# Kernel tuning notes

Measured on AMD Instinct MI355X. Metric: run time of the kernel, lower is better.

The kernel has to match this reference:

```python
import jax, jax.numpy as jnp
import numpy as np

EPS = 1e-5
NUM_HEADS = 8

def _inorm(x):
    # InstanceNorm1d (affine=False): normalize over last (length) axis per (B, C)
    m = x.mean(axis=-1, keepdims=True)
    v = x.var(axis=-1, keepdims=True)  # biased variance, as torch instance norm
    return (x - m) * jax.lax.rsqrt(v + EPS)

def setup_inputs() -> dict:
    key = jax.random.key(0)
    ks = jax.random.split(key, 12)
    B, Nl, HW = 4, 1024, 4096
    Cl, Cv, Ck, Cval, Cout = 512, 512, 256, 256, 256
    w = lambda k, shape: (jax.random.normal(k, shape, jnp.float32) * 0.02)
    return {
        "l": jax.random.normal(ks[0], (B, Nl, Cl), jnp.float32),
        "x": jax.random.normal(ks[1], (B, HW, Cv), jnp.float32),
        "Wq": w(ks[2], (Ck, Cl)),   "bq": w(ks[3], (Ck,)),
        "Wk": w(ks[4], (Ck, Cv)),   "bk": w(ks[5], (Ck,)),
        "Wv": w(ks[6], (Cval, Cv)), "bv": w(ks[7], (Cval,)),
        "Ww": w(ks[8], (Cout, Cval)), "bw": w(ks[9], (Cout,)),
    }

def reference(l, x, Wq, bq, Wk, bk, Wv, bv, Ww, bw):
    H = NUM_HEADS
    Ck = Wq.shape[0]
    Cv = Wv.shape[0]
    dk, dv = Ck // H, Cv // H
    B, Nl, _ = l.shape
    HW = x.shape[1]

    # 1x1 Conv1d == per-position linear
    q = jnp.einsum('blc,kc->blk', l, Wq) + bq                     # [B, Nl, Ck]
    k = jnp.einsum('bnc,kc->bkn', x, Wk) + bk[None, :, None]      # [B, Ck, HW]
    k = _inorm(k)                                                  # InstanceNorm over HW
    v = jnp.einsum('bnc,kc->bkn', x, Wv) + bv[None, :, None]      # [B, Cv, HW]

    q = q.reshape(B, Nl, H, dk).transpose(0, 2, 1, 3)             # [B, H, Nl, dk]
    k = k.reshape(B, H, dk, HW)                                   # [B, H, dk, HW]
    v = v.reshape(B, H, dv, HW)                                   # [B, H, dv, HW]

    sim = jnp.einsum('bhld,bhdn->bhln', q, k) * (Ck ** -0.5)      # [B, H, Nl, HW]
    att = jax.nn.softmax(sim, axis=-1)
    out = jnp.einsum('bhln,bhdn->bhld', att, v)                   # [B, H, Nl, dv]

    out = out.transpose(0, 2, 1, 3).reshape(B, Nl, Cv)            # [B, Nl, Cv]
    out = jnp.einsum('blc,oc->bol', out, Ww) + bw[None, :, None]  # [B, Cout, Nl]
    out = _inorm(out)                                              # InstanceNorm over Nl
    return out.transpose(0, 2, 1)                                  # [B, Nl, Cout]
```

## Files before the change

kernel.cpp:

```cpp
#include <hip/hip_runtime.h>

constexpr int Bn = 4, NL = 1024, HWn = 4096, NH = 8;

typedef __attribute__((ext_vector_type(8))) short bf16x8;
typedef __attribute__((ext_vector_type(4))) float f32x4;
#define MFMA16 __builtin_amdgcn_mfma_f32_16x16x32_bf16

extern "C" __device__ float __ocml_native_exp2_f32(float);

__device__ __forceinline__ float b2f(unsigned short u) {
  union { unsigned int i; float f; } x; x.i = ((unsigned int)u) << 16; return x.f;
}
__device__ __forceinline__ unsigned short f2b(float f) {
  union { float f; unsigned int i; } x; x.f = f;
  unsigned int r = x.i + 0x7fffu + ((x.i >> 16) & 1u);
  return (unsigned short)(r >> 16);
}

__device__ __forceinline__ void async_load16(const unsigned short* g, unsigned short* l) {
  __builtin_amdgcn_global_load_lds(
      (const __attribute__((address_space(1))) unsigned int*)g,
      (__attribute__((address_space(3))) unsigned int*)l, 16, 0, 0);
}

__global__ __launch_bounds__(256) void conv_bf16(const float* __restrict__ src,
    unsigned short* __restrict__ dst, int n)
{
  int i = (blockIdx.x * 256 + threadIdx.x) * 4;
  if (i < n) {
    float4 v = *(const float4*)(src + i);
    ushort4 o; o.x = f2b(v.x); o.y = f2b(v.y); o.z = f2b(v.z); o.w = f2b(v.w);
    *(ushort4*)(dst + i) = o;
  }
}

__global__ __launch_bounds__(256) void conv_w4(const float* __restrict__ Wk,
    const float* __restrict__ Wv, const float* __restrict__ Wq,
    const float* __restrict__ Ww,
    unsigned short* __restrict__ wkb, unsigned short* __restrict__ wvb,
    unsigned short* __restrict__ wqb,
    unsigned short* __restrict__ wwh, unsigned short* __restrict__ wwl)
{
  int i = (blockIdx.x * 256 + threadIdx.x) * 4;
  if (blockIdx.y == 3) {
    if (i >= 65536) return;
    float4 v = *(const float4*)(Ww + i);
    ushort4 hi, lo;
    hi.x = f2b(v.x); lo.x = f2b(v.x - b2f(hi.x));
    hi.y = f2b(v.y); lo.y = f2b(v.y - b2f(hi.y));
    hi.z = f2b(v.z); lo.z = f2b(v.z - b2f(hi.z));
    hi.w = f2b(v.w); lo.w = f2b(v.w - b2f(hi.w));
    *(ushort4*)(wwh + i) = hi;
    *(ushort4*)(wwl + i) = lo;
    return;
  }
  const float* src = blockIdx.y == 0 ? Wk : (blockIdx.y == 1 ? Wv : Wq);
  unsigned short* dst = blockIdx.y == 0 ? wkb : (blockIdx.y == 1 ? wvb : wqb);
  float4 v = *(const float4*)(src + i);
  ushort4 o; o.x = f2b(v.x); o.y = f2b(v.y); o.z = f2b(v.z); o.w = f2b(v.w);
  *(ushort4*)(dst + i) = o;
}

__global__ __launch_bounds__(256, 3) void gemm128(
    const unsigned short* __restrict__ xbf, const unsigned short* __restrict__ lbf,
    const unsigned short* __restrict__ wkb, const unsigned short* __restrict__ wvb,
    const unsigned short* __restrict__ wqb,
    const float* __restrict__ bk, const float* __restrict__ bv, const float* __restrict__ bq,
    unsigned short* __restrict__ khb, unsigned short* __restrict__ vhb,
    unsigned short* __restrict__ qbuf)
{
  __shared__ unsigned short As[2][4096];
  __shared__ unsigned short Bs[2][4096];
  const int id = blockIdx.x;
  const int mode = id < 256 ? 0 : (id < 512 ? 1 : 2);
  const int local = id - (mode == 0 ? 0 : (mode == 1 ? 256 : 512));
  const int rb = local >> 1, cb = local & 1;
  const int m0 = rb * 128, n0 = cb * 128;
  const unsigned short* A = (mode == 2) ? lbf : xbf;
  const unsigned short* W = (mode == 0) ? wkb : (mode == 1 ? wvb : wqb);
  const float* bias = (mode == 0) ? bk : (mode == 1 ? bv : bq);

  const int tid = threadIdx.x, w = tid >> 6, lane = tid & 63;
  const int quad = lane >> 4, l15 = lane & 15;
  const int wr = w >> 1, wc = w & 1;

  const int p0 = tid, p1 = tid + 256;
  const int am0 = p0 >> 2, ak0 = (p0 & 3) * 8;
  const int am1 = p1 >> 2, ak1 = (p1 & 3) * 8;

  f32x4 acc[4][4];
#pragma unroll
  for (int i = 0; i < 4; ++i)
#pragma unroll
    for (int j = 0; j < 4; ++j) acc[i][j] = (f32x4){0.f, 0.f, 0.f, 0.f};

  async_load16(A + (size_t)(m0 + am0) * 512 + ak0, &As[0][p0 * 8]);
  async_load16(A + (size_t)(m0 + am1) * 512 + ak1, &As[0][p1 * 8]);
  async_load16(W + (size_t)(n0 + am0) * 512 + ak0, &Bs[0][p0 * 8]);
  async_load16(W + (size_t)(n0 + am1) * 512 + ak1, &Bs[0][p1 * 8]);

  for (int kt = 0; kt < 16; ++kt) {
    const int cur = kt & 1;
    __syncthreads();
    if (kt < 15) {
      int k0 = (kt + 1) * 32;
      async_load16(A + (size_t)(m0 + am0) * 512 + k0 + ak0, &As[cur ^ 1][p0 * 8]);
      async_load16(A + (size_t)(m0 + am1) * 512 + k0 + ak1, &As[cur ^ 1][p1 * 8]);
      async_load16(W + (size_t)(n0 + am0) * 512 + k0 + ak0, &Bs[cur ^ 1][p0 * 8]);
      async_load16(W + (size_t)(n0 + am1) * 512 + k0 + ak1, &Bs[cur ^ 1][p1 * 8]);
    }
    bf16x8 af[4], bf[4];
#pragma unroll
    for (int fr = 0; fr < 4; ++fr)
      af[fr] = *(const bf16x8*)&As[cur][(wr * 64 + fr * 16 + l15) * 32 + quad * 8];
#pragma unroll
    for (int fc = 0; fc < 4; ++fc)
      bf[fc] = *(const bf16x8*)&Bs[cur][(wc * 64 + fc * 16 + l15) * 32 + quad * 8];
#pragma unroll
    for (int fr = 0; fr < 4; ++fr)
#pragma unroll
      for (int fc = 0; fc < 4; ++fc)
        acc[fr][fc] = MFMA16(af[fr], bf[fc], acc[fr][fc], 0, 0, 0);
  }

  float bb[4];
#pragma unroll
  for (int fc = 0; fc < 4; ++fc) bb[fc] = bias[n0 + wc * 64 + fc * 16 + l15];
  unsigned short* dst = (mode == 0) ? khb : (mode == 1 ? vhb : qbuf);
#pragma unroll
  for (int fr = 0; fr < 4; ++fr) {
#pragma unroll
    for (int fc = 0; fc < 4; ++fc) {
      int col = n0 + wc * 64 + fc * 16 + l15;
#pragma unroll
      for (int r = 0; r < 4; ++r) {
        int row = m0 + wr * 64 + fr * 16 + quad * 4 + r;
        unsigned short val = f2b(acc[fr][fc][r] + bb[fc]);
        if (mode == 2) {
          dst[(size_t)row * 256 + col] = val;
        } else {
          int b = row >> 12, n = row & 4095, h = col >> 5, d = col & 31;
          dst[((size_t)(b * 8 + h) * 4096 + n) * 32 + d] = val;
        }
      }
    }
  }
}

__global__ __launch_bounds__(256) void kvstats(const unsigned short* __restrict__ khb,
    const unsigned short* __restrict__ vhb,
    float* __restrict__ ksum, float* __restrict__ kss, float* __restrict__ vcs)
{
  const int which = blockIdx.x >> 5, bh = blockIdx.x & 31, seg = blockIdx.y;
  const int t = threadIdx.x, d = t & 31, g = t >> 5;
  __shared__ float rs[256], rss[256];
  if (which == 0) {
    const unsigned short* base = khb + (size_t)bh * 131072 + (size_t)seg * 512 * 32;
    float s = 0.f, ss = 0.f;
    for (int i = 0; i < 64; ++i) {
      float v = b2f(base[(size_t)(g + i * 8) * 32 + d]);
      s += v; ss += v * v;
    }
    rs[t] = s; rss[t] = ss;
    __syncthreads();
    if (t < 32) {
      float a = 0.f, b = 0.f;
      for (int g2 = 0; g2 < 8; ++g2) { a += rs[t + g2 * 32]; b += rss[t + g2 * 32]; }
      atomicAdd(&ksum[bh * 32 + t], a);
      atomicAdd(&kss[bh * 32 + t], b);
    }
  } else {
    const unsigned short* base = vhb + (size_t)bh * 131072 + (size_t)seg * 512 * 32;
    float s = 0.f;
    for (int i = 0; i < 64; ++i) s += b2f(base[(size_t)(g + i * 8) * 32 + d]);
    rs[t] = s;
    __syncthreads();
    if (t < 32) {
      float a = 0.f;
      for (int g2 = 0; g2 < 8; ++g2) a += rs[t + g2 * 32];
      vcs[seg * 1024 + bh * 32 + t] = a;
    }
  }
}

__global__ __launch_bounds__(256) void kfinal(const float* __restrict__ ksum,
    const float* __restrict__ kss, float* __restrict__ krstd)
{
  int i = blockIdx.x * 256 + threadIdx.x;
  float m = ksum[i] * (1.f / 4096.f);
  float var = kss[i] * (1.f / 4096.f) - m * m;
  krstd[i] = rsqrtf(var + 1e-5f);
}

__global__ __launch_bounds__(256) void vpack(const unsigned short* __restrict__ vh,
    unsigned short* __restrict__ vfrag)
{
  __shared__ unsigned short vt[256][42];
  const int bh = blockIdx.x >> 4, slab = blockIdx.x & 15;
  const unsigned short* src = vh + ((size_t)bh * 4096 + slab * 256) * 32;
  const int t = threadIdx.x;
#pragma unroll
  for (int i = 0; i < 4; ++i) {
    int p = i * 256 + t;
    int n = p >> 2, piece = p & 3;
    uint4 v = *(const uint4*)(src + (size_t)n * 32 + piece * 8);
    unsigned int* lrow = (unsigned int*)&vt[n][piece * 8];
    lrow[0] = v.x; lrow[1] = v.y; lrow[2] = v.z; lrow[3] = v.w;
  }
  __syncthreads();
#pragma unroll
  for (int i = 0; i < 4; ++i) {
    int op = i * 256 + t;
    int lanep = op & 63, rest = op >> 6;
    int dvt = rest & 1, kh2 = (rest >> 1) & 1, chunkl = rest >> 2;
    int lq = lanep >> 4, ll = lanep & 15;
    unsigned short o[8];
#pragma unroll
    for (int j = 0; j < 8; ++j) {
      int kappa = kh2 * 32 + lq * 8 + j;
      int nloc = (kappa >> 2) + 16 * (kappa & 3);
      o[j] = vt[chunkl * 64 + nloc][dvt * 16 + ll];
    }
    size_t dst = ((((size_t)bh * 64 + slab * 4 + chunkl) * 2 + kh2) * 2 + dvt) * 512 + lanep * 8;
    *(bf16x8*)(vfrag + dst) = *(const bf16x8*)o;
  }
}

__global__ __launch_bounds__(256, 4) void attn6(const unsigned short* __restrict__ qbuf,
    const unsigned short* __restrict__ khb, const unsigned short* __restrict__ vfrag,
    const float* __restrict__ krstd, const float* __restrict__ vcs,
    float* __restrict__ po, float* __restrict__ pd)
{
  const int bh = blockIdx.x, b = bh >> 3, h = bh & 7;
  const int lsuper = blockIdx.y, quarter = blockIdx.z;
  const int tid = threadIdx.x, w = tid >> 6, lane = tid & 63;
  const int quad = lane >> 4, l15 = lane & 15;

  __shared__ unsigned short kb_s[2][2048];
  __shared__ unsigned short vb_s[2][2048];
  __shared__ unsigned short ps[4][2][16][72];

  bf16x8 qa[2];
  {
    float fold[8];
    const float* rp = krstd + bh * 32 + quad * 8;
#pragma unroll
    for (int j = 0; j < 8; ++j) fold[j] = rp[j] * (0.0625f * 1.44269504f);
#pragma unroll
    for (int lf = 0; lf < 2; ++lf) {
      int l = lsuper * 128 + w * 32 + lf * 16 + l15;
      bf16x8 qr = *(const bf16x8*)(qbuf + ((size_t)(b * NL + l)) * 256 + h * 32 + quad * 8);
      const unsigned short* qq = (const unsigned short*)&qr;
      unsigned short tmp[8];
#pragma unroll
      for (int j = 0; j < 8; ++j) tmp[j] = f2b(b2f(qq[j]) * fold[j]);
      qa[lf] = *(const bf16x8*)tmp;
    }
  }

  float drow[2][4];
  f32x4 acc[2][2];
#pragma unroll
  for (int lf = 0; lf < 2; ++lf) {
#pragma unroll
    for (int r = 0; r < 4; ++r) drow[lf][r] = 0.f;
    acc[lf][0] = (f32x4){0.f,0.f,0.f,0.f};
    acc[lf][1] = (f32x4){0.f,0.f,0.f,0.f};
  }

  const unsigned short* kcbase = khb + (size_t)bh * 131072 + (size_t)quarter * 1024 * 32;
  const unsigned short* vcbase = vfrag + (size_t)bh * 131072 + (size_t)quarter * 16 * 2048;

  async_load16(kcbase + tid * 8, &kb_s[0][tid * 8]);
  async_load16(vcbase + tid * 8, &vb_s[0][tid * 8]);

  for (int c = 0; c < 16; ++c) {
    const int cur = c & 1;
    __syncthreads();
    if (c < 15) {
      async_load16(kcbase + (c + 1) * 2048 + tid * 8, &kb_s[cur ^ 1][tid * 8]);
      async_load16(vcbase + (c + 1) * 2048 + tid * 8, &vb_s[cur ^ 1][tid * 8]);
    }

    bf16x8 kb[4];
#pragma unroll
    for (int t = 0; t < 4; ++t)
      kb[t] = *(const bf16x8*)&kb_s[cur][(t * 16 + l15) * 32 + quad * 8];
    bf16x8 vb[4];
#pragma unroll
    for (int i = 0; i < 4; ++i)
      vb[i] = *(const bf16x8*)&vb_s[cur][i * 512 + lane * 8];

    f32x4 z = (f32x4){0.f,0.f,0.f,0.f};
#pragma unroll
    for (int lf = 0; lf < 2; ++lf) {
      f32x4 sv[4];
#pragma unroll
      for (int t = 0; t < 4; ++t) sv[t] = MFMA16(qa[lf], kb[t], z, 0, 0, 0);
#pragma unroll
      for (int r = 0; r < 4; ++r) {
        union { float f; unsigned int u; } e0, e1, e2, e3;
        float x0 = __ocml_native_exp2_f32(sv[0][r]);
        float x1 = __ocml_native_exp2_f32(sv[1][r]);
        float x2 = __ocml_native_exp2_f32(sv[2][r]);
        float x3 = __ocml_native_exp2_f32(sv[3][r]);
        drow[lf][r] += (x0 + x1) + (x2 + x3);
        e0.f = x0 - 1.0f; e1.f = x1 - 1.0f; e2.f = x2 - 1.0f; e3.f = x3 - 1.0f;
        uint2 pk;
        pk.x = (e0.u >> 16) | (e1.u & 0xFFFF0000u);
        pk.y = (e2.u >> 16) | (e3.u & 0xFFFF0000u);
        *(uint2*)&ps[w][lf][quad * 4 + r][l15 * 4] = pk;
      }
      asm volatile("s_waitcnt lgkmcnt(0)" ::: "memory");
#pragma unroll
      for (int kh2 = 0; kh2 < 2; ++kh2) {
        bf16x8 pa = *(const bf16x8*)&ps[w][lf][l15][kh2 * 32 + quad * 8];
#pragma unroll
        for (int dvt = 0; dvt < 2; ++dvt)
          acc[lf][dvt] = MFMA16(pa, vb[kh2 * 2 + dvt], acc[lf][dvt], 0, 0, 0);
      }
    }
  }

  const float* vc0 = vcs + (quarter * 2) * 1024 + bh * 32;
  const float* vc1 = vc0 + 1024;
  float cs0 = vc0[l15] + vc1[l15];
  float cs1 = vc0[16 + l15] + vc1[16 + l15];
#pragma unroll
  for (int lf = 0; lf < 2; ++lf)
#pragma unroll
    for (int r = 0; r < 4; ++r) {
      acc[lf][0][r] += cs0;
      acc[lf][1][r] += cs1;
    }

  const size_t PDo = (size_t)quarter * 32768 + (size_t)bh * 1024;
#pragma unroll
  for (int lf = 0; lf < 2; ++lf) {
#pragma unroll
    for (int r = 0; r < 4; ++r) {
      float sv = drow[lf][r];
      sv += __shfl_xor(sv, 1, 16);
      sv += __shfl_xor(sv, 2, 16);
      sv += __shfl_xor(sv, 4, 16);
      sv += __shfl_xor(sv, 8, 16);
      int l = lsuper * 128 + w * 32 + lf * 16 + quad * 4 + r;
      float2 val; val.x = acc[lf][0][r]; val.y = acc[lf][1][r];
      *(float2*)(po + (PDo + l) * 32 + l15 * 2) = val;
      if (l15 == 0) pd[PDo + l] = sv;
    }
  }
}

__global__ __launch_bounds__(256) void combine4(const float* __restrict__ po,
    const float* __restrict__ pd, unsigned short* __restrict__ aoh,
    unsigned short* __restrict__ aol)
{
  int gid = blockIdx.x * 256 + threadIdx.x;
  int dv = gid & 31, l = (gid >> 5) & (NL - 1), h = (gid >> 15) & 7, b = gid >> 18;
  int c = ((dv & 15) << 1) | (dv >> 4);
  size_t r = ((size_t)(b * 8 + h)) * 1024 + l;
  float d = 0.f, o = 0.f;
#pragma unroll
  for (int q = 0; q < 4; ++q) {
    size_t rr = (size_t)q * 32768 + r;
    d += pd[rr];
    o += po[rr * 32 + c];
  }
  o = o / d;
  unsigned short hi = f2b(o);
  size_t idx = ((size_t)(b * NL) + l) * 256 + h * 32 + dv;
  aoh[idx] = hi;
  aol[idx] = f2b(o - b2f(hi));
}

__global__ __launch_bounds__(256) void gemm_proj(
    const unsigned short* __restrict__ aoh, const unsigned short* __restrict__ aol,
    const unsigned short* __restrict__ wwh, const unsigned short* __restrict__ wwl,
    const float* __restrict__ bw, float* __restrict__ pj)
{
  __shared__ unsigned short As[64 * 32];
  __shared__ unsigned short Bs[128 * 32];
  const int bm = blockIdx.x * 64, bn = blockIdx.y * 128;
  const int tid = threadIdx.x, w = tid >> 6, lane = tid & 63;
  const int quad = lane >> 4, l15 = lane & 15;
  const int wr = w >> 1, wc = w & 1;
  const int arow = tid >> 2, apiece = (tid & 3) * 8;

  f32x4 acc[2][4];
#pragma unroll
  for (int i = 0; i < 2; ++i)
#pragma unroll
    for (int j = 0; j < 4; ++j) acc[i][j] = (f32x4){0.f, 0.f, 0.f, 0.f};

  for (int pair = 0; pair < 3; ++pair) {
    const unsigned short* A = (pair == 1) ? aol : aoh;
    const unsigned short* Bm = (pair == 2) ? wwl : wwh;
    for (int kt = 0; kt < 8; ++kt) {
      int k0 = kt * 32;
      __syncthreads();
      *(bf16x8*)&As[tid * 8] = *(const bf16x8*)(A + (size_t)(bm + arow) * 256 + k0 + apiece);
#pragma unroll
      for (int it = 0; it < 2; ++it) {
        int p = tid + it * 256;
        int brow = p >> 2, bpiece = (p & 3) * 8;
        *(bf16x8*)&Bs[p * 8] = *(const bf16x8*)(Bm + (size_t)(bn + brow) * 256 + k0 + bpiece);
      }
      __syncthreads();
      bf16x8 af[2], bf[4];
#pragma unroll
      for (int fr = 0; fr < 2; ++fr)
        af[fr] = *(const bf16x8*)&As[(wr * 32 + fr * 16 + l15) * 32 + quad * 8];
#pragma unroll
      for (int fc = 0; fc < 4; ++fc)
        bf[fc] = *(const bf16x8*)&Bs[(wc * 64 + fc * 16 + l15) * 32 + quad * 8];
#pragma unroll
      for (int fr = 0; fr < 2; ++fr)
#pragma unroll
        for (int fc = 0; fc < 4; ++fc)
          acc[fr][fc] = MFMA16(af[fr], bf[fc], acc[fr][fc], 0, 0, 0);
    }
  }

#pragma unroll
  for (int fr = 0; fr < 2; ++fr)
#pragma unroll
    for (int fc = 0; fc < 4; ++fc) {
      int col = bn + wc * 64 + fc * 16 + l15;
      float bb = bw[col];
#pragma unroll
      for (int r = 0; r < 4; ++r) {
        int row = bm + wr * 32 + fr * 16 + quad * 4 + r;
        pj[(size_t)row * 256 + col] = acc[fr][fc][r] + bb;
      }
    }
}

__global__ __launch_bounds__(256) void stats_kernel(const float* __restrict__ X,
    long batchStride, int rowsPerBlock,
    float* __restrict__ sum, float* __restrict__ sumsq)
{
  const int b = blockIdx.x, c = threadIdx.x;
  const long r0 = (long)blockIdx.y * rowsPerBlock;
  const float* base = X + (long)b * batchStride + r0 * 256 + c;
  float s = 0.f, ss = 0.f;
  for (int r = 0; r < rowsPerBlock; ++r) {
    float v = base[(long)r * 256];
    s += v; ss += v * v;
  }
  atomicAdd(&sum[b * 256 + c], s);
  atomicAdd(&sumsq[b * 256 + c], ss);
}

__global__ __launch_bounds__(256) void finalize_stats(const float* __restrict__ sum,
    const float* __restrict__ sumsq, float invR,
    float* __restrict__ mean, float* __restrict__ rstd)
{
  int i = blockIdx.x * 256 + threadIdx.x;
  float m = sum[i] * invR;
  float v = sumsq[i] * invR - m * m;
  mean[i] = m;
  rstd[i] = rsqrtf(v + 1e-5f);
}

__global__ __launch_bounds__(256) void final_out(const float* __restrict__ proj,
    const float* __restrict__ mean, const float* __restrict__ rstd,
    float* __restrict__ out)
{
  const int b = blockIdx.x, o = threadIdx.x;
  const int l1 = blockIdx.y * 16;
  const float m = mean[b * 256 + o], r = rstd[b * 256 + o];
  for (int i = 0; i < 16; ++i) {
    size_t idx = ((size_t)(b * NL + l1 + i)) * 256 + o;
    out[idx] = (proj[idx] - m) * r;
  }
}

extern "C" void kernel_launch(void* const* d_in, const int* in_sizes, int n_in,
                              void* d_out, int out_size, void* d_ws, size_t ws_size,
                              hipStream_t stream)
{
  const float* l  = (const float*)d_in[0];
  const float* x  = (const float*)d_in[1];
  const float* Wq = (const float*)d_in[2];
  const float* bq = (const float*)d_in[3];
  const float* Wk = (const float*)d_in[4];
  const float* bk = (const float*)d_in[5];
  const float* Wv = (const float*)d_in[6];
  const float* bv = (const float*)d_in[7];
  const float* Ww = (const float*)d_in[8];
  const float* bw = (const float*)d_in[9];
  float* out = (float*)d_out;

  unsigned short* up = (unsigned short*)d_ws;
  unsigned short* xbf   = up;
  unsigned short* lbf   = xbf   + 8388608;
  unsigned short* wkb   = lbf   + 2097152;
  unsigned short* wvb   = wkb   + 131072;
  unsigned short* wqb   = wvb   + 131072;
  unsigned short* qbuf  = wqb   + 131072;
  unsigned short* khb   = qbuf  + 1048576;
  unsigned short* vhb   = khb   + 4194304;
  unsigned short* vfrag = vhb   + 4194304;
  unsigned short* aoh   = vfrag + 4194304;
  unsigned short* aol   = aoh   + 1048576;
  unsigned short* wwh   = aol   + 1048576;
  unsigned short* wwl   = wwh   + 65536;
  float* F     = (float*)((char*)d_ws + 53477376);
  float* krstd = F;
  float* vcs   = krstd + 1024;
  float* po    = vcs + 8192;
  float* pd    = po + 4194304;
  float* pj    = pd + 131072;
  float* st    = pj + 1048576;
  float* ksum  = st;          float* kss   = st + 1024;
  float* psum  = st + 2048;   float* psq   = st + 3072;
  float* pmean = st + 4096;   float* prstd = st + 5120;

  hipMemsetAsync(st, 0, 4096 * sizeof(float), stream);

  dim3 blk(256);
  conv_bf16<<<8192, blk, 0, stream>>>(x,  xbf, 8388608);
  conv_bf16<<<2048, blk, 0, stream>>>(l,  lbf, 2097152);
  conv_w4<<<dim3(128, 4), blk, 0, stream>>>(Wk, Wv, Wq, Ww, wkb, wvb, wqb, wwh, wwl);
  gemm128<<<576, blk, 0, stream>>>(xbf, lbf, wkb, wvb, wqb, bk, bv, bq, khb, vhb, qbuf);
  kvstats<<<dim3(64, 8), blk, 0, stream>>>(khb, vhb, ksum, kss, vcs);
  kfinal<<<4, blk, 0, stream>>>(ksum, kss, krstd);
  vpack<<<512, blk, 0, stream>>>(vhb, vfrag);
  attn6<<<dim3(32, 8, 4), blk, 0, stream>>>(qbuf, khb, vfrag, krstd, vcs, po, pd);
  combine4<<<4096, blk, 0, stream>>>(po, pd, aoh, aol);
  gemm_proj<<<dim3(64, 2), blk, 0, stream>>>(aoh, aol, wwh, wwl, bw, pj);
  stats_kernel<<<dim3(4, 64), blk, 0, stream>>>(pj, (long)NL * 256, 16, psum, psq);
  finalize_stats<<<4, blk, 0, stream>>>(psum, psq, 1.0f / NL, pmean, prstd);
  final_out<<<dim3(4, 64), blk, 0, stream>>>(pj, pmean, prstd, out);
}
```

Baseline: 203.7 us.

## Merge conversion kernels, shrink attention P buffer, raise occupancy, use packed bf16 convert

The three fp32-to-bf16 conversion launches are merged into a single kernel that picks its source from a flat block index, removing two launches. In the attention kernel the per-wave P scratch in LDS is halved by sharing one buffer across both row fragments, and the launch-bounds occupancy hint goes from 4 to 6 blocks. The probability packing now uses a hardware packed bf16 conversion when available, which rounds instead of truncating. Reusing one P buffer for both fragments adds a write-after-read hazard between iterations, and the higher occupancy target may force register spills.

```diff
diff --git a/kernel.cpp b/kernel.cpp
--- a/kernel.cpp
+++ b/kernel.cpp
@@ -16,6 +16,16 @@
   unsigned int r = x.i + 0x7fffu + ((x.i >> 16) & 1u);
   return (unsigned short)(r >> 16);
 }
+__device__ __forceinline__ unsigned int pk_bf16(float lo, float hi) {
+#if __has_builtin(__builtin_amdgcn_cvt_pk_bf16_f32)
+  typedef __attribute__((ext_vector_type(2))) short bf16x2;
+  bf16x2 v = __builtin_amdgcn_cvt_pk_bf16_f32(lo, hi);
+  union { bf16x2 v; unsigned int u; } c; c.v = v; return c.u;
+#else
+  union { float f; unsigned int u; } a, b; a.f = lo; b.f = hi;
+  return (a.u >> 16) | (b.u & 0xFFFF0000u);
+#endif
+}
 
 __device__ __forceinline__ void async_load16(const unsigned short* g, unsigned short* l) {
   __builtin_amdgcn_global_load_lds(
@@ -23,27 +33,29 @@
       (__attribute__((address_space(3))) unsigned int*)l, 16, 0, 0);
 }
 
-__global__ __launch_bounds__(256) void conv_bf16(const float* __restrict__ src,
-    unsigned short* __restrict__ dst, int n)
-{
-  int i = (blockIdx.x * 256 + threadIdx.x) * 4;
-  if (i < n) {
+__global__ __launch_bounds__(256) void conv_all(const float* __restrict__ x,
+    const float* __restrict__ l, const float* __restrict__ Wk,
+    const float* __restrict__ Wv, const float* __restrict__ Wq,
+    const float* __restrict__ Ww,
+    unsigned short* __restrict__ xbf, unsigned short* __restrict__ lbf,
+    unsigned short* __restrict__ wkb, unsigned short* __restrict__ wvb,
+    unsigned short* __restrict__ wqb,
+    unsigned short* __restrict__ wwh, unsigned short* __restrict__ wwl)
+{
+  const int id = blockIdx.x;
+  if (id < 10624) {
+    const float* src; unsigned short* dst; int base;
+    if (id < 8192)       { src = x;  dst = xbf; base = id; }
+    else if (id < 10240) { src = l;  dst = lbf; base = id - 8192; }
+    else if (id < 10368) { src = Wk; dst = wkb; base = id - 10240; }
+    else if (id < 10496) { src = Wv; dst = wvb; base = id - 10368; }
+    else                 { src = Wq; dst = wqb; base = id - 10496; }
+    int i = (base * 256 + threadIdx.x) * 4;
     float4 v = *(const float4*)(src + i);
     ushort4 o; o.x = f2b(v.x); o.y = f2b(v.y); o.z = f2b(v.z); o.w = f2b(v.w);
     *(ushort4*)(dst + i) = o;
-  }
-}
-
-__global__ __launch_bounds__(256) void conv_w4(const float* __restrict__ Wk,
-    const float* __restrict__ Wv, const float* __restrict__ Wq,
-    const float* __restrict__ Ww,
-    unsigned short* __restrict__ wkb, unsigned short* __restrict__ wvb,
-    unsigned short* __restrict__ wqb,
-    unsigned short* __restrict__ wwh, unsigned short* __restrict__ wwl)
-{
-  int i = (blockIdx.x * 256 + threadIdx.x) * 4;
-  if (blockIdx.y == 3) {
-    if (i >= 65536) return;
+  } else {
+    int i = ((id - 10624) * 256 + threadIdx.x) * 4;
     float4 v = *(const float4*)(Ww + i);
     ushort4 hi, lo;
     hi.x = f2b(v.x); lo.x = f2b(v.x - b2f(hi.x));
@@ -52,13 +64,7 @@
     hi.w = f2b(v.w); lo.w = f2b(v.w - b2f(hi.w));
     *(ushort4*)(wwh + i) = hi;
     *(ushort4*)(wwl + i) = lo;
-    return;
-  }
-  const float* src = blockIdx.y == 0 ? Wk : (blockIdx.y == 1 ? Wv : Wq);
-  unsigned short* dst = blockIdx.y == 0 ? wkb : (blockIdx.y == 1 ? wvb : wqb);
-  float4 v = *(const float4*)(src + i);
-  ushort4 o; o.x = f2b(v.x); o.y = f2b(v.y); o.z = f2b(v.z); o.w = f2b(v.w);
-  *(ushort4*)(dst + i) = o;
+  }
 }
 
 __global__ __launch_bounds__(256, 3) void gemm128(
@@ -226,7 +232,7 @@
   }
 }
 
-__global__ __launch_bounds__(256, 4) void attn6(const unsigned short* __restrict__ qbuf,
+__global__ __launch_bounds__(256, 6) void attn7(const unsigned short* __restrict__ qbuf,
     const unsigned short* __restrict__ khb, const unsigned short* __restrict__ vfrag,
     const float* __restrict__ krstd, const float* __restrict__ vcs,
     float* __restrict__ po, float* __restrict__ pd)
@@ -238,7 +244,7 @@
 
   __shared__ unsigned short kb_s[2][2048];
   __shared__ unsigned short vb_s[2][2048];
-  __shared__ unsigned short ps[4][2][16][72];
+  __shared__ unsigned short ps[4][16][72];
 
   bf16x8 qa[2];
   {
@@ -299,22 +305,20 @@
       for (int t = 0; t < 4; ++t) sv[t] = MFMA16(qa[lf], kb[t], z, 0, 0, 0);
 #pragma unroll
       for (int r = 0; r < 4; ++r) {
-        union { float f; unsigned int u; } e0, e1, e2, e3;
         float x0 = __ocml_native_exp2_f32(sv[0][r]);
         float x1 = __ocml_native_exp2_f32(sv[1][r]);
         float x2 = __ocml_native_exp2_f32(sv[2][r]);
         float x3 = __ocml_native_exp2_f32(sv[3][r]);
         drow[lf][r] += (x0 + x1) + (x2 + x3);
-        e0.f = x0 - 1.0f; e1.f = x1 - 1.0f; e2.f = x2 - 1.0f; e3.f = x3 - 1.0f;
         uint2 pk;
-        pk.x = (e0.u >> 16) | (e1.u & 0xFFFF0000u);
-        pk.y = (e2.u >> 16) | (e3.u & 0xFFFF0000u);
-        *(uint2*)&ps[w][lf][quad * 4 + r][l15 * 4] = pk;
+        pk.x = pk_bf16(x0 - 1.0f, x1 - 1.0f);
+        pk.y = pk_bf16(x2 - 1.0f, x3 - 1.0f);
+        *(uint2*)&ps[w][quad * 4 + r][l15 * 4] = pk;
       }
       asm volatile("s_waitcnt lgkmcnt(0)" ::: "memory");
 #pragma unroll
       for (int kh2 = 0; kh2 < 2; ++kh2) {
-        bf16x8 pa = *(const bf16x8*)&ps[w][lf][l15][kh2 * 32 + quad * 8];
+        bf16x8 pa = *(const bf16x8*)&ps[w][l15][kh2 * 32 + quad * 8];
 #pragma unroll
         for (int dvt = 0; dvt < 2; ++dvt)
           acc[lf][dvt] = MFMA16(pa, vb[kh2 * 2 + dvt], acc[lf][dvt], 0, 0, 0);
@@ -520,14 +524,13 @@
   hipMemsetAsync(st, 0, 4096 * sizeof(float), stream);
 
   dim3 blk(256);
-  conv_bf16<<<8192, blk, 0, stream>>>(x,  xbf, 8388608);
-  conv_bf16<<<2048, blk, 0, stream>>>(l,  lbf, 2097152);
-  conv_w4<<<dim3(128, 4), blk, 0, stream>>>(Wk, Wv, Wq, Ww, wkb, wvb, wqb, wwh, wwl);
+  conv_all<<<10688, blk, 0, stream>>>(x, l, Wk, Wv, Wq, Ww,
+                                      xbf, lbf, wkb, wvb, wqb, wwh, wwl);
   gemm128<<<576, blk, 0, stream>>>(xbf, lbf, wkb, wvb, wqb, bk, bv, bq, khb, vhb, qbuf);
   kvstats<<<dim3(64, 8), blk, 0, stream>>>(khb, vhb, ksum, kss, vcs);
   kfinal<<<4, blk, 0, stream>>>(ksum, kss, krstd);
   vpack<<<512, blk, 0, stream>>>(vhb, vfrag);
-  attn6<<<dim3(32, 8, 4), blk, 0, stream>>>(qbuf, khb, vfrag, krstd, vcs, po, pd);
+  attn7<<<dim3(32, 8, 4), blk, 0, stream>>>(qbuf, khb, vfrag, krstd, vcs, po, pd);
   combine4<<<4096, blk, 0, stream>>>(po, pd, aoh, aol);
   gemm_proj<<<dim3(64, 2), blk, 0, stream>>>(aoh, aol, wwh, wwl, bw, pj);
   stats_kernel<<<dim3(4, 64), blk, 0, stream>>>(pj, (long)NL * 256, 16, psum, psq);
```

Result: slower. 228.8 us (+12.3%).
